# Performance work log

Measured on AMD Instinct MI355X. Metric: run time of the kernel, lower is better.

Reference implementation:

```python
import jax, jax.numpy as jnp
import numpy as np


def setup_inputs() -> dict:
    key = jax.random.key(0)
    ks = jax.random.split(key, 7)
    B = 4096
    x = jax.random.normal(ks[0], (B, 1, 28, 28), dtype=jnp.float32)
    # conv1: Conv2d(1, 32, 3), conv2: Conv2d(32, 64, 3)
    w1 = jax.random.normal(ks[1], (32, 1, 3, 3), dtype=jnp.float32) * 0.1
    b1 = jax.random.normal(ks[2], (32,), dtype=jnp.float32) * 0.1
    w2 = jax.random.normal(ks[3], (64, 32, 3, 3), dtype=jnp.float32) * 0.05
    b2 = jax.random.normal(ks[4], (64,), dtype=jnp.float32) * 0.05
    # fc1: Linear(9216, 128), fc2: Linear(128, 10)
    fc1_w = jax.random.normal(ks[5], (128, 9216), dtype=jnp.float32) * 0.01
    fc1_b = jnp.zeros((128,), dtype=jnp.float32)
    fc2_w = jax.random.normal(ks[6], (10, 128), dtype=jnp.float32) * 0.05
    fc2_b = jnp.zeros((10,), dtype=jnp.float32)
    return {"x": x, "w1": w1, "b1": b1, "w2": w2, "b2": b2,
            "fc1_w": fc1_w, "fc1_b": fc1_b, "fc2_w": fc2_w, "fc2_b": fc2_b}


def _conv_valid(x, w, b):
    # The original FFTConv1d (flatten-to-1D FFT circular correlation + roll +
    # crop) is mathematically identical to valid cross-correlation (nn.Conv2d).
    y = jax.lax.conv_general_dilated(
        x, w, window_strides=(1, 1), padding="VALID",
        dimension_numbers=("NCHW", "OIHW", "NCHW"))
    return y + b[None, :, None, None]


def reference(x, w1, b1, w2, b2, fc1_w, fc1_b, fc2_w, fc2_b):
    h = jax.nn.relu(_conv_valid(x, w1, b1))        # [B,32,26,26]
    h = jax.nn.relu(_conv_valid(h, w2, b2))        # [B,64,24,24]
    B, C, H, W = h.shape
    h = h.reshape(B, C, H // 2, 2, W // 2, 2).max(axis=(3, 5))  # maxpool 2x2 -> [B,64,12,12]
    # dropout layers are identity at inference
    h = h.reshape(B, -1)                           # [B,9216], C-major like torch.flatten
    h = jax.nn.relu(h @ fc1_w.T + fc1_b)           # [B,128]
    logits = h @ fc2_w.T + fc2_b                   # [B,10]
    # original computes log_softmax but returns the pre-softmax logits
    return logits
```

## Files before the change

### kernel.cpp

```cpp
#include <hip/hip_runtime.h>
#include <hip/hip_bf16.h>
#include <string.h>

using short8 = __attribute__((ext_vector_type(8))) short;
using f32x4  = __attribute__((ext_vector_type(4))) float;
using f32x2  = __attribute__((ext_vector_type(2))) float;

#define POOLN     9216
#define FC1N      128
#define WT2_ELEMS 18432
#define WT2_BYTES 36864
#define H1S_STRIDE 36
#define XS_STRIDE  29

#define GLL16(gp, lp) __builtin_amdgcn_global_load_lds( \
    (const __attribute__((address_space(1))) void*)(gp), \
    (__attribute__((address_space(3))) void*)(lp), 16, 0, 0)

static __device__ __forceinline__ unsigned short f2bf(float f) {
  unsigned int u = __builtin_bit_cast(unsigned int, f);
  unsigned int r = (u + 0x7FFFu + ((u >> 16) & 1u)) >> 16;
  return (unsigned short)r;
}

static __device__ __forceinline__ unsigned int pkbf(float lo, float hi) {
  __hip_bfloat162 h2 = __float22bfloat162_rn(make_float2(lo, hi));
  unsigned int r;
  memcpy(&r, &h2, sizeof(r));
  return r;
}

__global__ __launch_bounds__(256) void k_wt2(const float* __restrict__ w2,
    unsigned short* __restrict__ wt2) {
  int idx = blockIdx.x * 256 + threadIdx.x;
  if (idx >= WT2_ELEMS) return;
  int j = idx & 7;
  int l = (idx >> 3) & 63;
  int tn = idx >> 9;
  int tap = tn >> 2, n = tn & 3;
  int oc = n * 16 + (l & 15);
  int ic = (l >> 4) * 8 + j;
  wt2[idx] = f2bf(w2[oc * 288 + ic * 9 + tap]);
}

__global__ __launch_bounds__(256) void k_fw1t(const float* __restrict__ w,
    unsigned short* __restrict__ wt) {
  int c = blockIdx.x;
  __shared__ float row[9216];
  int t = threadIdx.x;
  const float* src = w + (size_t)c * 9216;
  for (int i = t; i < 9216; i += 256) row[i] = src[i];
  __syncthreads();
  unsigned short* dst = wt + (size_t)c * 9216;
  for (int k = t; k < 9216; k += 256) {
    int sp = k >> 6, oc = k & 63;
    dst[k] = f2bf(row[oc * 144 + sp]);
  }
}

__global__ __launch_bounds__(256, 4) void kc_fused(const float* __restrict__ x,
    const float* __restrict__ w1, const float* __restrict__ b1,
    const unsigned short* __restrict__ wt2, const float* __restrict__ b2,
    unsigned short* __restrict__ pooled) {
  int img = blockIdx.x;
  int tt = blockIdx.y;
  __shared__ float xs[12 * XS_STRIDE];
  __shared__ __align__(16) unsigned short h1s[260 * H1S_STRIDE];
  int t = threadIdx.x;
  int wv = t >> 6, ln = t & 63;
  int r0x = tt * 8;

  const float* xp = x + (size_t)img * 784 + (size_t)r0x * 28;
  for (int i = t; i < 12 * 28; i += 256) {
    int r = i / 28, c = i - r * 28;
    xs[r * XS_STRIDE + c] = xp[r * 28 + c];
  }

  int wvu = __builtin_amdgcn_readfirstlane(wv);
  f32x2 wp[4][9], bp[4];
  #pragma unroll
  for (int p = 0; p < 4; ++p) {
    int o = wvu * 8 + p * 2;
    bp[p] = (f32x2){b1[o], b1[o + 1]};
    #pragma unroll
    for (int q = 0; q < 9; ++q)
      wp[p][q] = (f32x2){w1[o * 9 + q], w1[(o + 1) * 9 + q]};
  }
  __syncthreads();

  if (ln < 52) {
    int half = (ln >= 26);
    int xcol = ln - half * 26;
    int y0 = half * 5;
    float win[3][3];
    #pragma unroll
    for (int c = 0; c < 3; ++c) {
      win[1][c] = xs[(y0 + 0) * XS_STRIDE + xcol + c];
      win[2][c] = xs[(y0 + 1) * XS_STRIDE + xcol + c];
    }
    #pragma unroll
    for (int i = 0; i < 5; ++i) {
      #pragma unroll
      for (int c = 0; c < 3; ++c) {
        win[0][c] = win[1][c];
        win[1][c] = win[2][c];
        win[2][c] = xs[(y0 + i + 2) * XS_STRIDE + xcol + c];
      }
      f32x2 s[4] = {bp[0], bp[1], bp[2], bp[3]};
      #pragma unroll
      for (int r = 0; r < 3; ++r)
        #pragma unroll
        for (int c = 0; c < 3; ++c) {
          f32x2 wv2 = (f32x2){win[r][c], win[r][c]};
          #pragma unroll
          for (int p = 0; p < 4; ++p)
            s[p] = __builtin_elementwise_fma(wv2, wp[p][r * 3 + c], s[p]);
        }
      unsigned int packed[4];
      const f32x2 z2 = (f32x2){0.f, 0.f};
      #pragma unroll
      for (int p = 0; p < 4; ++p) {
        f32x2 sp = __builtin_elementwise_max(s[p], z2);
        packed[p] = pkbf(sp.x, sp.y);
      }
      int pos = (y0 + i) * 26 + xcol;
      unsigned short* dst = &h1s[pos * H1S_STRIDE + wv * 8];
      *(uint2*)dst = make_uint2(packed[0], packed[1]);
      *(uint2*)(dst + 4) = make_uint2(packed[2], packed[3]);
    }
  }
  __syncthreads();

  int col = ln & 15;
  int g = (ln >> 4) & 3;

  int abase[3];
  #pragma unroll
  for (int i = 0; i < 3; ++i) {
    int y = 2 * wv + (col & 1);
    int xx = 8 * i + (col >> 1);
    abase[i] = (y * 26 + xx) * (H1S_STRIDE * 2) + g * 16;
  }

  f32x4 acc[3][4];
  #pragma unroll
  for (int m = 0; m < 3; ++m)
    #pragma unroll
    for (int n = 0; n < 4; ++n)
      acc[m][n] = (f32x4){0.f, 0.f, 0.f, 0.f};

  const char* hsb = (const char*)h1s;
  #pragma unroll
  for (int tap = 0; tap < 9; ++tap) {
    int ky = tap / 3, kx = tap - ky * 3;
    int toff = (ky * 26 + kx) * (H1S_STRIDE * 2);
    short8 bf[4];
    #pragma unroll
    for (int n = 0; n < 4; ++n)
      bf[n] = *(const short8*)(wt2 + ((size_t)(tap * 4 + n) * 64 + ln) * 8);
    #pragma unroll
    for (int m = 0; m < 3; ++m) {
      union { short8 v; uint2 d[2]; } af;
      af.d[0] = *(const uint2*)(hsb + abase[m] + toff);
      af.d[1] = *(const uint2*)(hsb + abase[m] + toff + 8);
      #pragma unroll
      for (int n = 0; n < 4; ++n)
        acc[m][n] = __builtin_amdgcn_mfma_f32_16x16x32_bf16(af.v, bf[n], acc[m][n], 0, 0, 0);
    }
  }

  float bias[4];
  #pragma unroll
  for (int n = 0; n < 4; ++n) bias[n] = b2[n * 16 + col];
  unsigned short* pp = pooled + (size_t)img * POOLN;
  int pr = tt * 4 + wv;
  #pragma unroll
  for (int m = 0; m < 3; ++m) {
    int sp = pr * 12 + m * 4 + g;
    float rv[4];
    #pragma unroll
    for (int n = 0; n < 4; ++n) {
      f32x4 a = acc[m][n];
      float v = fmaxf(fmaxf(a[0], a[1]), fmaxf(a[2], a[3]));
      rv[n] = fmaxf(v + bias[n], 0.f);
    }
    unsigned int p01 = pkbf(rv[0], rv[1]);
    unsigned int p23 = pkbf(rv[2], rv[3]);
    unsigned short* pr0 = pp + sp * 64 + col;
    pr0[0]  = (unsigned short)p01;
    pr0[16] = (unsigned short)(p01 >> 16);
    pr0[32] = (unsigned short)p23;
    pr0[48] = (unsigned short)(p23 >> 16);
  }
}

__global__ __launch_bounds__(256) void k3_fc1_mfma(
    const unsigned short* __restrict__ a, const unsigned short* __restrict__ w,
    float* __restrict__ part, int nrpad) {
  __shared__ __align__(16) unsigned short As[2][4096];
  __shared__ __align__(16) unsigned short Bs[2][8192];
  int row0 = blockIdx.x * 64;
  int kbase = blockIdx.y * 2304;
  int t = threadIdx.x;
  int wv = t >> 6, l = t & 63;
  int rsub = l >> 3;
  int src_sw = ((l & 7) ^ rsub) << 4;

  const char* abase = (const char*)a + (size_t)row0 * 18432;
  const char* bbase = (const char*)w;

  auto stage = [&](int buf, int step) {
    size_t k0b = (size_t)(kbase + step * 64) * 2;
    #pragma unroll
    for (int i = 0; i < 2; ++i) {
      int c = wv * 2 + i;
      GLL16(abase + (size_t)(c * 8 + rsub) * 18432 + k0b + src_sw,
            (char*)As[buf] + c * 1024);
    }
    #pragma unroll
    for (int i = 0; i < 4; ++i) {
      int c = wv * 4 + i;
      GLL16(bbase + (size_t)(c * 8 + rsub) * 18432 + k0b + src_sw,
            (char*)Bs[buf] + c * 1024);
    }
  };

  int wm = wv >> 1, wn = wv & 1;
  int lr = l & 15, g2 = l >> 4;
  int rdxor = (lr & 7) << 4;

  f32x4 acc[2][4];
  #pragma unroll
  for (int mf = 0; mf < 2; ++mf)
    #pragma unroll
    for (int nf = 0; nf < 4; ++nf)
      acc[mf][nf] = (f32x4){0.f, 0.f, 0.f, 0.f};

  stage(0, 0);
  __syncthreads();
  for (int s = 0; s < 36; ++s) {
    int cur = s & 1;
    if (s < 35) stage(cur ^ 1, s + 1);
    const char* Ab = (const char*)As[cur];
    const char* Bb = (const char*)Bs[cur];
    #pragma unroll
    for (int ksub = 0; ksub < 2; ++ksub) {
      int koff = (ksub * 64 + g2 * 16) ^ rdxor;
      short8 af0 = *(const short8*)(Ab + (wm * 32 + lr) * 128 + koff);
      short8 af1 = *(const short8*)(Ab + (wm * 32 + 16 + lr) * 128 + koff);
      short8 bf[4];
      #pragma unroll
      for (int nf = 0; nf < 4; ++nf)
        bf[nf] = *(const short8*)(Bb + (wn * 64 + nf * 16 + lr) * 128 + koff);
      #pragma unroll
      for (int nf = 0; nf < 4; ++nf) {
        acc[0][nf] = __builtin_amdgcn_mfma_f32_16x16x32_bf16(af0, bf[nf], acc[0][nf], 0, 0, 0);
        acc[1][nf] = __builtin_amdgcn_mfma_f32_16x16x32_bf16(af1, bf[nf], acc[1][nf], 0, 0, 0);
      }
    }
    __syncthreads();
  }

  float* pp = part + (size_t)blockIdx.y * nrpad * 128 + (size_t)row0 * 128;
  #pragma unroll
  for (int mf = 0; mf < 2; ++mf)
    #pragma unroll
    for (int nf = 0; nf < 4; ++nf)
      #pragma unroll
      for (int rr = 0; rr < 4; ++rr) {
        int r = wm * 32 + mf * 16 + g2 * 4 + rr;
        int c = wn * 64 + nf * 16 + lr;
        pp[r * 128 + c] = acc[mf][nf][rr];
      }
}

__global__ __launch_bounds__(256) void k_tail(const float* __restrict__ part,
    const float* __restrict__ fb1, const float* __restrict__ fw2,
    const float* __restrict__ fb2, float* __restrict__ out,
    int nr, int nrpad) {
  __shared__ float sh[2][128];
  int t = threadIdx.x;
  int r = t >> 7, c = t & 127;
  int row = blockIdx.x * 2 + r;
  size_t stride = (size_t)nrpad * 128;
  if (row < nr) {
    size_t i = (size_t)row * 128 + c;
    float s = part[i] + part[stride + i] + part[2 * stride + i] + part[3 * stride + i];
    sh[r][c] = fmaxf(s + fb1[c], 0.f);
  }
  __syncthreads();
  if (t < 20) {
    int rr = t / 10, j = t - rr * 10;
    int orow = blockIdx.x * 2 + rr;
    if (orow < nr) {
      const float4* hv = (const float4*)sh[rr];
      const float4* wv = (const float4*)(fw2 + (size_t)j * 128);
      float s = 0.f;
      #pragma unroll
      for (int q = 0; q < 32; ++q) {
        float4 h4 = hv[q];
        float4 w4 = wv[q];
        s = fmaf(h4.x, w4.x, s);
        s = fmaf(h4.y, w4.y, s);
        s = fmaf(h4.z, w4.z, s);
        s = fmaf(h4.w, w4.w, s);
      }
      out[(size_t)orow * 10 + j] = s + fb2[j];
    }
  }
}

extern "C" void kernel_launch(void* const* d_in, const int* in_sizes, int n_in,
                              void* d_out, int out_size, void* d_ws, size_t ws_size,
                              hipStream_t stream) {
  const float* x   = (const float*)d_in[0];
  const float* w1  = (const float*)d_in[1];
  const float* b1  = (const float*)d_in[2];
  const float* w2  = (const float*)d_in[3];
  const float* b2  = (const float*)d_in[4];
  const float* fw1 = (const float*)d_in[5];
  const float* fb1 = (const float*)d_in[6];
  const float* fw2 = (const float*)d_in[7];
  const float* fb2 = (const float*)d_in[8];
  float* out = (float*)d_out;

  const int B = in_sizes[0] / 784;

  unsigned short* wt2 = (unsigned short*)d_ws;
  unsigned short* fw1t = (unsigned short*)((char*)d_ws + WT2_BYTES);
  const size_t carve = WT2_BYTES + (size_t)9216 * 128 * 2;
  char* base = (char*)d_ws + carve;
  size_t avail = (ws_size > carve) ? ws_size - carve : 0;
  const size_t per_img = (size_t)POOLN * 2 + 2048;
  int Bc = (int)(avail / per_img);
  if (Bc > B) Bc = B;
  Bc &= ~63;
  if (Bc < 64) Bc = 64;

  unsigned short* pooled = (unsigned short*)base;
  float* part = (float*)(base + (size_t)Bc * (POOLN * 2));

  k_wt2<<<(WT2_ELEMS + 255) / 256, 256, 0, stream>>>(w2, wt2);
  k_fw1t<<<128, 256, 0, stream>>>(fw1, fw1t);

  for (int i0 = 0; i0 < B; i0 += Bc) {
    int nr = (B - i0 < Bc) ? (B - i0) : Bc;
    int mtiles = (nr + 63) / 64;
    int nrpad = mtiles * 64;
    kc_fused<<<dim3(nr, 3), 256, 0, stream>>>(x + (size_t)i0 * 784, w1, b1,
                                              wt2, b2, pooled);
    k3_fc1_mfma<<<dim3(mtiles, 4), 256, 0, stream>>>(pooled, fw1t, part, nrpad);
    k_tail<<<(nr + 1) / 2, 256, 0, stream>>>(part, fb1, fw2, fb2,
                                             out + (size_t)i0 * 10, nr, nrpad);
  }
}
```

Before: 156.0 us.

## Process four images per conv block with double-buffered conv1/conv2 software pipeline

The fused conv kernel now handles four images per block. It double-buffers the conv1 activation tile in shared memory so that conv2 MFMA work on one image is interleaved with conv1 compute for the next. The input staging through shared memory is removed and conv1 reads x directly from global memory. Weight and bias register setup is amortized across images and block count drops by four. The launch grid uses nr/IPB, which assumes nr is divisible by 4, and the launch-bounds occupancy hint is lowered to 3.

```diff
diff --git a/kernel.cpp b/kernel.cpp
--- a/kernel.cpp
+++ b/kernel.cpp
@@ -11,7 +11,7 @@
 #define WT2_ELEMS 18432
 #define WT2_BYTES 36864
 #define H1S_STRIDE 36
-#define XS_STRIDE  29
+#define IPB       4
 
 #define GLL16(gp, lp) __builtin_amdgcn_global_load_lds( \
     (const __attribute__((address_space(1))) void*)(gp), \
@@ -58,24 +58,17 @@
   }
 }
 
-__global__ __launch_bounds__(256, 4) void kc_fused(const float* __restrict__ x,
+__global__ __launch_bounds__(256, 3) void kc_pipe(const float* __restrict__ x,
     const float* __restrict__ w1, const float* __restrict__ b1,
     const unsigned short* __restrict__ wt2, const float* __restrict__ b2,
     unsigned short* __restrict__ pooled) {
-  int img = blockIdx.x;
+  int g0 = blockIdx.x * IPB;
   int tt = blockIdx.y;
-  __shared__ float xs[12 * XS_STRIDE];
-  __shared__ __align__(16) unsigned short h1s[260 * H1S_STRIDE];
+  __shared__ __align__(16) unsigned short h1s[2][260 * H1S_STRIDE];
   int t = threadIdx.x;
   int wv = t >> 6, ln = t & 63;
   int r0x = tt * 8;
 
-  const float* xp = x + (size_t)img * 784 + (size_t)r0x * 28;
-  for (int i = t; i < 12 * 28; i += 256) {
-    int r = i / 28, c = i - r * 28;
-    xs[r * XS_STRIDE + c] = xp[r * 28 + c];
-  }
-
   int wvu = __builtin_amdgcn_readfirstlane(wv);
   f32x2 wp[4][9], bp[4];
   #pragma unroll
@@ -86,17 +79,33 @@
     for (int q = 0; q < 9; ++q)
       wp[p][q] = (f32x2){w1[o * 9 + q], w1[(o + 1) * 9 + q]};
   }
-  __syncthreads();
-
-  if (ln < 52) {
-    int half = (ln >= 26);
-    int xcol = ln - half * 26;
-    int y0 = half * 5;
+
+  int half = (ln >= 26);
+  int xcolr = ln - half * 26;
+  int xcol = xcolr > 25 ? 25 : xcolr;
+  bool c1act = (ln < 52);
+  int y0 = half * 5;
+
+  int col = ln & 15;
+  int g = (ln >> 4) & 3;
+  int abase[3];
+  #pragma unroll
+  for (int i = 0; i < 3; ++i) {
+    int y = 2 * wv + (col & 1);
+    int xx = 8 * i + (col >> 1);
+    abase[i] = (y * 26 + xx) * (H1S_STRIDE * 2) + g * 16;
+  }
+  float bias[4];
+  #pragma unroll
+  for (int n = 0; n < 4; ++n) bias[n] = b2[n * 16 + col];
+
+  auto conv1_body = [&](int img, int buf) {
+    const float* xg = x + (size_t)img * 784 + (size_t)r0x * 28;
     float win[3][3];
     #pragma unroll
     for (int c = 0; c < 3; ++c) {
-      win[1][c] = xs[(y0 + 0) * XS_STRIDE + xcol + c];
-      win[2][c] = xs[(y0 + 1) * XS_STRIDE + xcol + c];
+      win[1][c] = xg[(y0 + 0) * 28 + xcol + c];
+      win[2][c] = xg[(y0 + 1) * 28 + xcol + c];
     }
     #pragma unroll
     for (int i = 0; i < 5; ++i) {
@@ -104,7 +113,7 @@
       for (int c = 0; c < 3; ++c) {
         win[0][c] = win[1][c];
         win[1][c] = win[2][c];
-        win[2][c] = xs[(y0 + i + 2) * XS_STRIDE + xcol + c];
+        win[2][c] = xg[(y0 + i + 2) * 28 + xcol + c];
       }
       f32x2 s[4] = {bp[0], bp[1], bp[2], bp[3]};
       #pragma unroll
@@ -123,75 +132,72 @@
         f32x2 sp = __builtin_elementwise_max(s[p], z2);
         packed[p] = pkbf(sp.x, sp.y);
       }
-      int pos = (y0 + i) * 26 + xcol;
-      unsigned short* dst = &h1s[pos * H1S_STRIDE + wv * 8];
-      *(uint2*)dst = make_uint2(packed[0], packed[1]);
-      *(uint2*)(dst + 4) = make_uint2(packed[2], packed[3]);
-    }
-  }
+      if (c1act) {
+        int pos = (y0 + i) * 26 + xcol;
+        unsigned short* dst = &h1s[buf][pos * H1S_STRIDE + wv * 8];
+        *(uint2*)dst = make_uint2(packed[0], packed[1]);
+        *(uint2*)(dst + 4) = make_uint2(packed[2], packed[3]);
+      }
+    }
+  };
+
+  auto conv2_body = [&](int img, int buf) {
+    const char* hsb = (const char*)h1s[buf];
+    f32x4 acc[3][4];
+    #pragma unroll
+    for (int m = 0; m < 3; ++m)
+      #pragma unroll
+      for (int n = 0; n < 4; ++n)
+        acc[m][n] = (f32x4){0.f, 0.f, 0.f, 0.f};
+    #pragma unroll
+    for (int tap = 0; tap < 9; ++tap) {
+      int ky = tap / 3, kx = tap - ky * 3;
+      int toff = (ky * 26 + kx) * (H1S_STRIDE * 2);
+      short8 bf[4];
+      #pragma unroll
+      for (int n = 0; n < 4; ++n)
+        bf[n] = *(const short8*)(wt2 + ((size_t)(tap * 4 + n) * 64 + ln) * 8);
+      #pragma unroll
+      for (int m = 0; m < 3; ++m) {
+        union { short8 v; uint2 d[2]; } af;
+        af.d[0] = *(const uint2*)(hsb + abase[m] + toff);
+        af.d[1] = *(const uint2*)(hsb + abase[m] + toff + 8);
+        #pragma unroll
+        for (int n = 0; n < 4; ++n)
+          acc[m][n] = __builtin_amdgcn_mfma_f32_16x16x32_bf16(af.v, bf[n], acc[m][n], 0, 0, 0);
+      }
+    }
+    unsigned short* pp = pooled + (size_t)img * POOLN;
+    int pr = tt * 4 + wv;
+    #pragma unroll
+    for (int m = 0; m < 3; ++m) {
+      int sp = pr * 12 + m * 4 + g;
+      float rv[4];
+      #pragma unroll
+      for (int n = 0; n < 4; ++n) {
+        f32x4 a = acc[m][n];
+        float v = fmaxf(fmaxf(a[0], a[1]), fmaxf(a[2], a[3]));
+        rv[n] = fmaxf(v + bias[n], 0.f);
+      }
+      unsigned int p01 = pkbf(rv[0], rv[1]);
+      unsigned int p23 = pkbf(rv[2], rv[3]);
+      unsigned short* pr0 = pp + sp * 64 + col;
+      pr0[0]  = (unsigned short)p01;
+      pr0[16] = (unsigned short)(p01 >> 16);
+      pr0[32] = (unsigned short)p23;
+      pr0[48] = (unsigned short)(p23 >> 16);
+    }
+  };
+
+  conv1_body(g0, 0);
   __syncthreads();
-
-  int col = ln & 15;
-  int g = (ln >> 4) & 3;
-
-  int abase[3];
-  #pragma unroll
-  for (int i = 0; i < 3; ++i) {
-    int y = 2 * wv + (col & 1);
-    int xx = 8 * i + (col >> 1);
-    abase[i] = (y * 26 + xx) * (H1S_STRIDE * 2) + g * 16;
-  }
-
-  f32x4 acc[3][4];
-  #pragma unroll
-  for (int m = 0; m < 3; ++m)
-    #pragma unroll
-    for (int n = 0; n < 4; ++n)
-      acc[m][n] = (f32x4){0.f, 0.f, 0.f, 0.f};
-
-  const char* hsb = (const char*)h1s;
-  #pragma unroll
-  for (int tap = 0; tap < 9; ++tap) {
-    int ky = tap / 3, kx = tap - ky * 3;
-    int toff = (ky * 26 + kx) * (H1S_STRIDE * 2);
-    short8 bf[4];
-    #pragma unroll
-    for (int n = 0; n < 4; ++n)
-      bf[n] = *(const short8*)(wt2 + ((size_t)(tap * 4 + n) * 64 + ln) * 8);
-    #pragma unroll
-    for (int m = 0; m < 3; ++m) {
-      union { short8 v; uint2 d[2]; } af;
-      af.d[0] = *(const uint2*)(hsb + abase[m] + toff);
-      af.d[1] = *(const uint2*)(hsb + abase[m] + toff + 8);
-      #pragma unroll
-      for (int n = 0; n < 4; ++n)
-        acc[m][n] = __builtin_amdgcn_mfma_f32_16x16x32_bf16(af.v, bf[n], acc[m][n], 0, 0, 0);
-    }
-  }
-
-  float bias[4];
-  #pragma unroll
-  for (int n = 0; n < 4; ++n) bias[n] = b2[n * 16 + col];
-  unsigned short* pp = pooled + (size_t)img * POOLN;
-  int pr = tt * 4 + wv;
-  #pragma unroll
-  for (int m = 0; m < 3; ++m) {
-    int sp = pr * 12 + m * 4 + g;
-    float rv[4];
-    #pragma unroll
-    for (int n = 0; n < 4; ++n) {
-      f32x4 a = acc[m][n];
-      float v = fmaxf(fmaxf(a[0], a[1]), fmaxf(a[2], a[3]));
-      rv[n] = fmaxf(v + bias[n], 0.f);
-    }
-    unsigned int p01 = pkbf(rv[0], rv[1]);
-    unsigned int p23 = pkbf(rv[2], rv[3]);
-    unsigned short* pr0 = pp + sp * 64 + col;
-    pr0[0]  = (unsigned short)p01;
-    pr0[16] = (unsigned short)(p01 >> 16);
-    pr0[32] = (unsigned short)p23;
-    pr0[48] = (unsigned short)(p23 >> 16);
-  }
+  #pragma unroll
+  for (int i = 1; i < IPB; ++i) {
+    conv2_body(g0 + i - 1, (i - 1) & 1);
+    conv1_body(g0 + i, i & 1);
+    __syncthreads();
+  }
+  conv2_body(g0 + IPB - 1, (IPB - 1) & 1);
 }
 
 __global__ __launch_bounds__(256) void k3_fc1_mfma(
@@ -347,8 +353,8 @@
     int nr = (B - i0 < Bc) ? (B - i0) : Bc;
     int mtiles = (nr + 63) / 64;
     int nrpad = mtiles * 64;
-    kc_fused<<<dim3(nr, 3), 256, 0, stream>>>(x + (size_t)i0 * 784, w1, b1,
-                                              wt2, b2, pooled);
+    kc_pipe<<<dim3(nr / IPB, 3), 256, 0, stream>>>(x + (size_t)i0 * 784, w1, b1,
+                                                   wt2, b2, pooled);
     k3_fc1_mfma<<<dim3(mtiles, 4), 256, 0, stream>>>(pooled, fw1t, part, nrpad);
     k_tail<<<(nr + 1) / 2, 256, 0, stream>>>(part, fb1, fw2, fb2,
                                              out + (size_t)i0 * 10, nr, nrpad);
```

After: 181.3 us. +16.2%, slower.
